# Optimization experiments

Measured on AMD Instinct MI355X. Metric: run time of the kernel, lower is better.

## Reference

```python
import jax, jax.numpy as jnp
import numpy as np

DIM = 2048
N_HEADS = 32
N_KV_HEADS = 8
HEAD_DIM = 64
N_REP = N_HEADS // N_KV_HEADS
SEQ = 2048
BATCH = 1


def _llama3_scaled_rope(head_dim, end, base=10000.0, scale_factor=8):
    # matches executorch precompute_freqs_cis with use_scaled=True
    freqs = 1.0 / (base ** (np.arange(0, head_dim, 2)[: head_dim // 2] / head_dim))
    low_freq_factor, high_freq_factor, old_ctx = 1.0, 4.0, 8192.0
    low_wl = old_ctx / low_freq_factor
    high_wl = old_ctx / high_freq_factor
    wavelen = 2.0 * np.pi / freqs
    smooth = (old_ctx / wavelen - low_freq_factor) / (high_freq_factor - low_freq_factor)
    scaled = np.where(
        wavelen < high_wl,
        freqs,
        np.where(wavelen > low_wl, freqs / scale_factor,
                 (1.0 - smooth) * freqs / scale_factor + smooth * freqs),
    )
    t = np.arange(end, dtype=np.float64)
    ang = np.outer(t, scaled)
    return np.cos(ang).astype(np.float32), np.sin(ang).astype(np.float32)


def setup_inputs() -> dict:
    key = jax.random.key(0)
    kx, kq, kk, kv, ko = jax.random.split(key, 5)
    x = jax.random.normal(kx, (BATCH, SEQ, DIM), dtype=jnp.float32)
    sc = 0.02
    wq = jax.random.normal(kq, (N_HEADS * HEAD_DIM, DIM), dtype=jnp.float32) * sc
    wk = jax.random.normal(kk, (N_KV_HEADS * HEAD_DIM, DIM), dtype=jnp.float32) * sc
    wv = jax.random.normal(kv, (N_KV_HEADS * HEAD_DIM, DIM), dtype=jnp.float32) * sc
    wo = jax.random.normal(ko, (N_HEADS * HEAD_DIM, DIM), dtype=jnp.float32).T * sc
    cos, sin = _llama3_scaled_rope(HEAD_DIM, SEQ)
    return {"x": x, "freqs_cos": jnp.asarray(cos), "freqs_sin": jnp.asarray(sin),
            "wq": wq, "wk": wk, "wv": wv, "wo": wo}


def _apply_rotary(x, cos, sin):
    # x: [b, s, h, hd]; cos/sin: [s, hd//2]; interleaved-pair RoPE
    xr = x[..., 0::2]
    xi = x[..., 1::2]
    c = cos[None, :, None, :]
    s = sin[None, :, None, :]
    out_r = xr * c - xi * s
    out_i = xr * s + xi * c
    return jnp.stack([out_r, out_i], axis=-1).reshape(x.shape)


def reference(x, freqs_cos, freqs_sin, wq, wk, wv, wo):
    b, s, _ = x.shape
    q = (x @ wq.T).reshape(b, s, N_HEADS, HEAD_DIM)
    k = (x @ wk.T).reshape(b, s, N_KV_HEADS, HEAD_DIM)
    v = (x @ wv.T).reshape(b, s, N_KV_HEADS, HEAD_DIM)
    q = _apply_rotary(q, freqs_cos, freqs_sin)
    k = _apply_rotary(k, freqs_cos, freqs_sin)
    # [b, h, s, hd]
    q = q.transpose(0, 2, 1, 3)
    k = k.transpose(0, 2, 1, 3)
    v = v.transpose(0, 2, 1, 3)
    # GQA: repeat_interleave over head dim
    k = jnp.repeat(k, N_REP, axis=1)
    v = jnp.repeat(v, N_REP, axis=1)
    scale = 1.0 / jnp.sqrt(jnp.asarray(HEAD_DIM, dtype=x.dtype))
    scores = jnp.einsum("bhqd,bhkd->bhqk", q, k) * scale
    causal = jnp.tril(jnp.ones((s, s), dtype=bool))
    scores = jnp.where(causal[None, None], scores, jnp.finfo(scores.dtype).min)
    attn = jax.nn.softmax(scores, axis=-1)
    y = jnp.einsum("bhqk,bhkd->bhqd", attn, v)
    y = y.transpose(0, 2, 1, 3).reshape(b, s, N_HEADS * HEAD_DIM)
    return y @ wo.T
```

## Files before the change

kernel.cpp:

```cpp
#include <hip/hip_runtime.h>
#include <hip/hip_bf16.h>

typedef __attribute__((ext_vector_type(8))) __bf16 bf16x8;
typedef __attribute__((ext_vector_type(4))) __bf16 bf16x4;
typedef __attribute__((ext_vector_type(4))) float f32x4;

#define DIM 2048
#define SEQ 2048
#define NH 32
#define NKV 8
#define HD 64
#define QKVD 3072
#define KOFF 2048
#define VOFF 2560
#define KVDIM 512

__device__ __forceinline__ void gld16(const __bf16* g, __bf16* l) {
    __builtin_amdgcn_global_load_lds(
        (const __attribute__((address_space(1))) void*)g,
        (__attribute__((address_space(3))) void*)l, 16, 0, 0);
}

__global__ void cvt_f32_bf16(const float* __restrict__ in, __bf16* __restrict__ out, int n4) {
    int i = blockIdx.x * blockDim.x + threadIdx.x;
    if (i < n4) {
        float4 v = reinterpret_cast<const float4*>(in)[i];
        bf16x4 o;
        o[0] = (__bf16)v.x; o[1] = (__bf16)v.y; o[2] = (__bf16)v.z; o[3] = (__bf16)v.w;
        reinterpret_cast<bf16x4*>(out)[i] = o;
    }
}

__global__ __launch_bounds__(256) void transpose_v(const __bf16* __restrict__ V,
                                                   __bf16* __restrict__ VT) {
    __shared__ __bf16 t[64][72];
    const int tid = threadIdx.x;
    const int r = tid >> 2, c0 = (tid & 3) * 16;
    const int sb = blockIdx.x * 64;
    const int db = blockIdx.y * 64;
    bf16x8 a0 = *reinterpret_cast<const bf16x8*>(V + (size_t)(sb + r) * QKVD + db + c0);
    bf16x8 a1 = *reinterpret_cast<const bf16x8*>(V + (size_t)(sb + r) * QKVD + db + c0 + 8);
#pragma unroll
    for (int e = 0; e < 8; ++e) { t[c0 + e][r] = a0[e]; t[c0 + 8 + e][r] = a1[e]; }
    __syncthreads();
    bf16x8 o0 = *reinterpret_cast<const bf16x8*>(&t[r][c0]);
    bf16x8 o1 = *reinterpret_cast<const bf16x8*>(&t[r][c0 + 8]);
    *reinterpret_cast<bf16x8*>(VT + (size_t)(db + r) * SEQ + sb + c0) = o0;
    *reinterpret_cast<bf16x8*>(VT + (size_t)(db + r) * SEQ + sb + c0 + 8) = o1;
}

template <typename OutT, bool ROPE>
__global__ __launch_bounds__(256) void gemm_tn(const __bf16* __restrict__ A,
                                               const __bf16* __restrict__ B,
                                               OutT* __restrict__ C,
                                               int M, int N, int K,
                                               float scale, int scaleNlim,
                                               const float* __restrict__ fc,
                                               const float* __restrict__ fs) {
    __shared__ __align__(16) __bf16 As[2][2][128 * 32];
    __shared__ __align__(16) __bf16 Bs[2][2][64 * 32];
    const int tid = threadIdx.x;
    const int lane = tid & 63;
    const int w = tid >> 6;
    const int l15 = lane & 15, lhi = lane >> 4;
    const int mb = blockIdx.y * 128;
    const int nb = blockIdx.x * 64;
    const int wm = (w >> 1) * 64, wn = (w & 1) * 32;

    const int srow = lane >> 2, scol = (lane & 3) * 8;
    const __bf16* gA0 = A + (size_t)(mb + w * 16 + srow) * K + scol;
    const __bf16* gA1 = A + (size_t)(mb + (w + 4) * 16 + srow) * K + scol;
    const __bf16* gB0 = B + (size_t)(nb + w * 16 + srow) * K + scol;

    auto stage = [&](int kk, int buf) {
#pragma unroll
        for (int s = 0; s < 2; ++s) {
            gld16(gA0 + kk + s * 32, As[buf][s] + w * 512);
            gld16(gA1 + kk + s * 32, As[buf][s] + (w + 4) * 512);
            gld16(gB0 + kk + s * 32, Bs[buf][s] + w * 512);
        }
    };

    stage(0, 0);
    __syncthreads();

    f32x4 acc[4][2] = {};
    int cur = 0;
    for (int kk = 0; kk < K; kk += 64, cur ^= 1) {
        if (kk + 64 < K) stage(kk + 64, cur ^ 1);
#pragma unroll
        for (int s = 0; s < 2; ++s) {
            bf16x8 a[4], b[2];
#pragma unroll
            for (int i = 0; i < 4; ++i)
                a[i] = *reinterpret_cast<const bf16x8*>(&As[cur][s][(wm + i * 16 + l15) * 32 + lhi * 8]);
#pragma unroll
            for (int j = 0; j < 2; ++j)
                b[j] = *reinterpret_cast<const bf16x8*>(&Bs[cur][s][(wn + j * 16 + l15) * 32 + lhi * 8]);
#pragma unroll
            for (int i = 0; i < 4; ++i)
#pragma unroll
                for (int j = 0; j < 2; ++j)
                    acc[i][j] = __builtin_amdgcn_mfma_f32_16x16x32_bf16(a[i], b[j], acc[i][j], 0, 0, 0);
        }
        __syncthreads();
    }

    const float sc = (nb < scaleNlim) ? scale : 1.0f;
    const bool doRope = ROPE && (nb < VOFF);
#pragma unroll
    for (int i = 0; i < 4; ++i)
#pragma unroll
        for (int j = 0; j < 2; ++j)
#pragma unroll
            for (int r = 0; r < 4; ++r) {
                float v = acc[i][j][r] * sc;
                if (doRope) {
                    const int col = nb + wn + j * 16 + l15;
                    const int row = mb + wm + i * 16 + lhi * 4 + r;
                    const float vp = __shfl_xor(v, 1);
                    const int fi = (col & 63) >> 1;
                    const float cc = fc[row * 32 + fi];
                    const float ss = fs[row * 32 + fi];
                    v = (col & 1) ? (vp * ss + v * cc) : (v * cc - vp * ss);
                }
                C[(size_t)(mb + wm + i * 16 + lhi * 4 + r) * N + nb + wn + j * 16 + l15] = (OutT)v;
            }
}

__global__ __launch_bounds__(256) void attn_kernel(const __bf16* __restrict__ QKV,
                                                   const __bf16* __restrict__ VT,
                                                   __bf16* __restrict__ Y) {
    const int bx = blockIdx.x;
    const int p = bx >> 5;
    const int h = bx & 31;
    const int kvh = h >> 2;
    const int tid = threadIdx.x;
    const int lane = tid & 63;
    const int w = tid >> 6;
    const int l15 = lane & 15, lhi = lane >> 4;

    __shared__ __align__(16) __bf16 Kl[2][128 * 64];
    __shared__ __align__(16) __bf16 Vl[2][64 * 128];
    __shared__ __align__(16) __bf16 Pl[4][16 * 128];

    const __bf16* Qp = QKV + h * HD;
    const __bf16* Kp = QKV + KOFF + kvh * HD;
    const __bf16* Vth = VT + (size_t)(kvh * HD) * SEQ;

    const int ksr = lane >> 3;
    const int ksc = ((lane & 7) ^ ksr) * 8;
    const int vsr = lane >> 4;

    auto stage = [&](int jt, int buf) {
        const int kvb = jt * 128;
#pragma unroll
        for (int c = 0; c < 4; ++c) {
            const int rb = w * 32 + c * 8;
            gld16(Kp + (size_t)(kvb + rb + ksr) * QKVD + ksc, &Kl[buf][rb * 64]);
        }
#pragma unroll
        for (int c = 0; c < 4; ++c) {
            const int db = w * 16 + c * 4;
            const int row = db + vsr;
            const int col = ((lane & 15) ^ (row & 7)) * 8;
            gld16(Vth + (size_t)row * SEQ + kvb + col, &Vl[buf][db * 128]);
        }
    };

    const int pkey = (l15 & 7) << 2;

    for (int seg = 0; seg < 2; ++seg) {
        const int qt = seg ? (31 - p) : p;
        const int qb = qt * 64;
        const int nkt = (qt + 2) >> 1;
        const int qrow = qb + w * 16 + l15;

        const __bf16* qptr = Qp + (size_t)qrow * QKVD;
        bf16x8 qf0 = *reinterpret_cast<const bf16x8*>(qptr + lhi * 8);
        bf16x8 qf1 = *reinterpret_cast<const bf16x8*>(qptr + 32 + lhi * 8);

        f32x4 o[4] = {};
        float mrun = -1e30f;
        float lpart = 0.f;

        stage(0, 0);
        __syncthreads();

        int cur = 0;
        for (int j = 0; j < nkt; ++j, cur ^= 1) {
            const bool pre = (j + 1 < nkt);
            if (pre) stage(j + 1, cur ^ 1);

            f32x4 sacc[8];
            __builtin_amdgcn_s_setprio(1);
#pragma unroll
            for (int t = 0; t < 8; ++t) {
                const int row = t * 16 + l15;
                const int key = row & 7;
                bf16x8 kf0 = *reinterpret_cast<const bf16x8*>(
                    &Kl[cur][row * 64 + ((lhi ^ key) * 8)]);
                bf16x8 kf1 = *reinterpret_cast<const bf16x8*>(
                    &Kl[cur][row * 64 + (((4 + lhi) ^ key) * 8)]);
                f32x4 z = {0.f, 0.f, 0.f, 0.f};
                z = __builtin_amdgcn_mfma_f32_16x16x32_bf16(kf0, qf0, z, 0, 0, 0);
                z = __builtin_amdgcn_mfma_f32_16x16x32_bf16(kf1, qf1, z, 0, 0, 0);
                sacc[t] = z;
            }
            __builtin_amdgcn_s_setprio(0);

            if (j == nkt - 1) {
#pragma unroll
                for (int t = 0; t < 8; ++t)
#pragma unroll
                    for (int r = 0; r < 4; ++r) {
                        const int kv = j * 128 + t * 16 + lhi * 4 + r;
                        if (kv > qrow) sacc[t][r] = -1e30f;
                    }
            }

            float mt[8];
#pragma unroll
            for (int t = 0; t < 8; ++t)
                mt[t] = fmaxf(fmaxf(sacc[t][0], sacc[t][1]),
                              fmaxf(sacc[t][2], sacc[t][3]));
            float pm = fmaxf(fmaxf(fmaxf(mt[0], mt[1]), fmaxf(mt[2], mt[3])),
                             fmaxf(fmaxf(mt[4], mt[5]), fmaxf(mt[6], mt[7])));

            if (!__all(pm - mrun <= 8.0f)) {
                float full = pm;
                full = fmaxf(full, __shfl_xor(full, 16));
                full = fmaxf(full, __shfl_xor(full, 32));
                const float mn = fmaxf(mrun, full);
                const float a = exp2f(mrun - mn);
                mrun = mn;
                lpart *= a;
                float ar[4];
#pragma unroll
                for (int r = 0; r < 4; ++r) ar[r] = __shfl(a, lhi * 4 + r);
#pragma unroll
                for (int t = 0; t < 4; ++t)
#pragma unroll
                    for (int r = 0; r < 4; ++r) o[t][r] *= ar[r];
            }

#pragma unroll
            for (int t = 0; t < 8; ++t) {
                bf16x4 pk;
#pragma unroll
                for (int r = 0; r < 4; ++r) {
                    const float pv = exp2f(sacc[t][r] - mrun);
                    lpart += pv;
                    pk[r] = (__bf16)pv;
                }
                const int sw = (t * 4 + lhi) ^ pkey;
                *reinterpret_cast<bf16x4*>(&Pl[w][l15 * 128 + sw * 4]) = pk;
            }

            bf16x8 pf[4];
#pragma unroll
            for (int c = 0; c < 4; ++c) {
                const int s0 = (c * 8 + lhi * 2) ^ pkey;
                pf[c] = *reinterpret_cast<const bf16x8*>(&Pl[w][l15 * 128 + s0 * 4]);
            }
            __builtin_amdgcn_s_setprio(1);
#pragma unroll
            for (int t = 0; t < 4; ++t) {
                const int row = t * 16 + l15;
                const int key = row & 7;
#pragma unroll
                for (int c = 0; c < 4; ++c) {
                    bf16x8 vf = *reinterpret_cast<const bf16x8*>(
                        &Vl[cur][row * 128 + (((c * 4 + lhi) ^ key) * 8)]);
                    o[t] = __builtin_amdgcn_mfma_f32_16x16x32_bf16(pf[c], vf, o[t], 0, 0, 0);
                }
            }
            __builtin_amdgcn_s_setprio(0);

            __syncthreads();
        }

        float ls = lpart;
        ls += __shfl_xor(ls, 16);
        ls += __shfl_xor(ls, 32);
        float lr[4];
#pragma unroll
        for (int r = 0; r < 4; ++r) lr[r] = __shfl(ls, lhi * 4 + r);
#pragma unroll
        for (int t = 0; t < 4; ++t)
#pragma unroll
            for (int r = 0; r < 4; ++r) {
                const float val = o[t][r] / lr[r];
                Y[(size_t)(qb + w * 16 + lhi * 4 + r) * DIM + h * HD + t * 16 + l15] =
                    (__bf16)val;
            }
    }
}

extern "C" void kernel_launch(void* const* d_in, const int* in_sizes, int n_in,
                              void* d_out, int out_size, void* d_ws, size_t ws_size,
                              hipStream_t stream) {
    const float* x    = (const float*)d_in[0];
    const float* fcos = (const float*)d_in[1];
    const float* fsin = (const float*)d_in[2];
    const float* wq   = (const float*)d_in[3];
    const float* wk   = (const float*)d_in[4];
    const float* wv   = (const float*)d_in[5];
    const float* wo   = (const float*)d_in[6];
    float* out = (float*)d_out;

    __bf16* xb    = (__bf16*)d_ws;
    __bf16* wqkvb = xb + (size_t)SEQ * DIM;
    __bf16* wob   = wqkvb + (size_t)QKVD * DIM;
    __bf16* QKVb  = wob + (size_t)DIM * DIM;
    __bf16* Yb    = QKVb + (size_t)SEQ * QKVD;
    __bf16* VTb   = Yb + (size_t)SEQ * DIM;

    const int nx  = SEQ * DIM / 4;
    const int nw  = DIM * DIM / 4;
    const int nkv = KVDIM * DIM / 4;
    cvt_f32_bf16<<<(nx + 255) / 256, 256, 0, stream>>>(x, xb, nx);
    cvt_f32_bf16<<<(nw + 255) / 256, 256, 0, stream>>>(wq, wqkvb, nw);
    cvt_f32_bf16<<<(nkv + 255) / 256, 256, 0, stream>>>(wk, wqkvb + (size_t)KOFF * DIM, nkv);
    cvt_f32_bf16<<<(nkv + 255) / 256, 256, 0, stream>>>(wv, wqkvb + (size_t)VOFF * DIM, nkv);
    cvt_f32_bf16<<<(nw + 255) / 256, 256, 0, stream>>>(wo, wob, nw);

    gemm_tn<__bf16, true><<<dim3(QKVD / 64, SEQ / 128), 256, 0, stream>>>(
        xb, wqkvb, QKVb, SEQ, QKVD, DIM, 0.125f * 1.4426950408889634f, KOFF, fcos, fsin);

    transpose_v<<<dim3(SEQ / 64, KVDIM / 64), 256, 0, stream>>>(QKVb + VOFF, VTb);

    attn_kernel<<<dim3(512), 256, 0, stream>>>(QKVb, VTb, Yb);

    gemm_tn<float, false><<<dim3(DIM / 64, SEQ / 128), 256, 0, stream>>>(
        Yb, wob, out, SEQ, DIM, DIM, 1.0f, 0, nullptr, nullptr);
}
```

Measured before the change: 151.0 us.

## Split attention into one q-tile per block with 64-wide KV tiles

Each attention block now handles a single 64-row query tile instead of a paired causal segment. The grid doubles to 1024 blocks, ordered so that heavy tiles are scheduled first. KV tiles shrink from 128 to 64 keys, which halves the LDS footprint, and launch bounds request 4 blocks per CU. This aims to improve occupancy and load balance, and the causal mask now wastes less work on the diagonal tile. In exchange there are more loop iterations, more barriers, and Q is reloaded per block.

```diff
diff --git a/kernel.cpp b/kernel.cpp
--- a/kernel.cpp
+++ b/kernel.cpp
@@ -128,173 +128,160 @@
             }
 }
 
-__global__ __launch_bounds__(256) void attn_kernel(const __bf16* __restrict__ QKV,
-                                                   const __bf16* __restrict__ VT,
-                                                   __bf16* __restrict__ Y) {
+__global__ __launch_bounds__(256, 4) void attn_kernel(const __bf16* __restrict__ QKV,
+                                                      const __bf16* __restrict__ VT,
+                                                      __bf16* __restrict__ Y) {
     const int bx = blockIdx.x;
-    const int p = bx >> 5;
+    const int g = bx >> 8;
+    const int a = (bx >> 5) & 7;
     const int h = bx & 31;
+    const int qt = (g == 0) ? 31 - a : (g == 1) ? a : (g == 2) ? 23 - a : 8 + a;
     const int kvh = h >> 2;
     const int tid = threadIdx.x;
     const int lane = tid & 63;
     const int w = tid >> 6;
     const int l15 = lane & 15, lhi = lane >> 4;
 
-    __shared__ __align__(16) __bf16 Kl[2][128 * 64];
-    __shared__ __align__(16) __bf16 Vl[2][64 * 128];
-    __shared__ __align__(16) __bf16 Pl[4][16 * 128];
+    __shared__ __align__(16) __bf16 Kl[2][64 * 64];
+    __shared__ __align__(16) __bf16 Vl[2][64 * 64];
+    __shared__ __align__(16) __bf16 Pl[4][16 * 64];
 
     const __bf16* Qp = QKV + h * HD;
     const __bf16* Kp = QKV + KOFF + kvh * HD;
     const __bf16* Vth = VT + (size_t)(kvh * HD) * SEQ;
 
-    const int ksr = lane >> 3;
-    const int ksc = ((lane & 7) ^ ksr) * 8;
-    const int vsr = lane >> 4;
+    const int sr = lane >> 3;
+    const int ksc = ((lane & 7) ^ sr) * 8;
+    const int rswz = (l15 & 7);
 
     auto stage = [&](int jt, int buf) {
-        const int kvb = jt * 128;
-#pragma unroll
-        for (int c = 0; c < 4; ++c) {
-            const int rb = w * 32 + c * 8;
-            gld16(Kp + (size_t)(kvb + rb + ksr) * QKVD + ksc, &Kl[buf][rb * 64]);
-        }
-#pragma unroll
-        for (int c = 0; c < 4; ++c) {
-            const int db = w * 16 + c * 4;
-            const int row = db + vsr;
-            const int col = ((lane & 15) ^ (row & 7)) * 8;
-            gld16(Vth + (size_t)row * SEQ + kvb + col, &Vl[buf][db * 128]);
+        const int kvb = jt * 64;
+#pragma unroll
+        for (int c = 0; c < 2; ++c) {
+            const int row = w * 16 + c * 8;
+            gld16(Kp + (size_t)(kvb + row + sr) * QKVD + ksc, &Kl[buf][row * 64]);
+            gld16(Vth + (size_t)(row + sr) * SEQ + kvb + ksc, &Vl[buf][row * 64]);
         }
     };
 
-    const int pkey = (l15 & 7) << 2;
-
-    for (int seg = 0; seg < 2; ++seg) {
-        const int qt = seg ? (31 - p) : p;
-        const int qb = qt * 64;
-        const int nkt = (qt + 2) >> 1;
-        const int qrow = qb + w * 16 + l15;
-
-        const __bf16* qptr = Qp + (size_t)qrow * QKVD;
-        bf16x8 qf0 = *reinterpret_cast<const bf16x8*>(qptr + lhi * 8);
-        bf16x8 qf1 = *reinterpret_cast<const bf16x8*>(qptr + 32 + lhi * 8);
-
-        f32x4 o[4] = {};
-        float mrun = -1e30f;
-        float lpart = 0.f;
-
-        stage(0, 0);
+    const int qb = qt * 64;
+    const int qrow = qb + w * 16 + l15;
+
+    const __bf16* qptr = Qp + (size_t)qrow * QKVD;
+    bf16x8 qf0 = *reinterpret_cast<const bf16x8*>(qptr + lhi * 8);
+    bf16x8 qf1 = *reinterpret_cast<const bf16x8*>(qptr + 32 + lhi * 8);
+
+    f32x4 o[4] = {};
+    float mrun = -1e30f;
+    float lpart = 0.f;
+
+    const int pkey = (l15 & 7) << 1;
+
+    stage(0, 0);
+    __syncthreads();
+
+    int cur = 0;
+    for (int j = 0; j <= qt; ++j, cur ^= 1) {
+        const bool pre = (j < qt);
+        if (pre) stage(j + 1, cur ^ 1);
+
+        f32x4 sacc[4];
+        __builtin_amdgcn_s_setprio(1);
+#pragma unroll
+        for (int t = 0; t < 4; ++t) {
+            const int rb = (t * 16 + l15) * 64;
+            bf16x8 kf0 = *reinterpret_cast<const bf16x8*>(
+                &Kl[cur][rb + ((lhi ^ rswz) * 8)]);
+            bf16x8 kf1 = *reinterpret_cast<const bf16x8*>(
+                &Kl[cur][rb + (((4 + lhi) ^ rswz) * 8)]);
+            f32x4 z = {0.f, 0.f, 0.f, 0.f};
+            z = __builtin_amdgcn_mfma_f32_16x16x32_bf16(kf0, qf0, z, 0, 0, 0);
+            z = __builtin_amdgcn_mfma_f32_16x16x32_bf16(kf1, qf1, z, 0, 0, 0);
+            sacc[t] = z;
+        }
+        __builtin_amdgcn_s_setprio(0);
+
+        if (j == qt) {
+#pragma unroll
+            for (int t = 0; t < 4; ++t)
+#pragma unroll
+                for (int r = 0; r < 4; ++r) {
+                    const int kv = j * 64 + t * 16 + lhi * 4 + r;
+                    if (kv > qrow) sacc[t][r] = -1e30f;
+                }
+        }
+
+        float mt[4];
+#pragma unroll
+        for (int t = 0; t < 4; ++t)
+            mt[t] = fmaxf(fmaxf(sacc[t][0], sacc[t][1]),
+                          fmaxf(sacc[t][2], sacc[t][3]));
+        const float pm = fmaxf(fmaxf(mt[0], mt[1]), fmaxf(mt[2], mt[3]));
+
+        if (!__all(pm - mrun <= 8.0f)) {
+            float full = pm;
+            full = fmaxf(full, __shfl_xor(full, 16));
+            full = fmaxf(full, __shfl_xor(full, 32));
+            const float mn = fmaxf(mrun, full);
+            const float aa = exp2f(mrun - mn);
+            mrun = mn;
+            lpart *= aa;
+            float ar[4];
+#pragma unroll
+            for (int r = 0; r < 4; ++r) ar[r] = __shfl(aa, lhi * 4 + r);
+#pragma unroll
+            for (int t = 0; t < 4; ++t)
+#pragma unroll
+                for (int r = 0; r < 4; ++r) o[t][r] *= ar[r];
+        }
+
+#pragma unroll
+        for (int t = 0; t < 4; ++t) {
+            bf16x4 pk;
+#pragma unroll
+            for (int r = 0; r < 4; ++r) {
+                const float pv = exp2f(sacc[t][r] - mrun);
+                lpart += pv;
+                pk[r] = (__bf16)pv;
+            }
+            const int sw = (t * 4 + lhi) ^ pkey;
+            *reinterpret_cast<bf16x4*>(&Pl[w][l15 * 64 + sw * 4]) = pk;
+        }
+
+        bf16x8 pf0 = *reinterpret_cast<const bf16x8*>(
+            &Pl[w][l15 * 64 + (((lhi * 2) ^ pkey) * 4)]);
+        bf16x8 pf1 = *reinterpret_cast<const bf16x8*>(
+            &Pl[w][l15 * 64 + (((8 + lhi * 2) ^ pkey) * 4)]);
+        __builtin_amdgcn_s_setprio(1);
+#pragma unroll
+        for (int t = 0; t < 4; ++t) {
+            const int rb = (t * 16 + l15) * 64;
+            bf16x8 vf0 = *reinterpret_cast<const bf16x8*>(
+                &Vl[cur][rb + ((lhi ^ rswz) * 8)]);
+            bf16x8 vf1 = *reinterpret_cast<const bf16x8*>(
+                &Vl[cur][rb + (((4 + lhi) ^ rswz) * 8)]);
+            o[t] = __builtin_amdgcn_mfma_f32_16x16x32_bf16(pf0, vf0, o[t], 0, 0, 0);
+            o[t] = __builtin_amdgcn_mfma_f32_16x16x32_bf16(pf1, vf1, o[t], 0, 0, 0);
+        }
+        __builtin_amdgcn_s_setprio(0);
+
         __syncthreads();
-
-        int cur = 0;
-        for (int j = 0; j < nkt; ++j, cur ^= 1) {
-            const bool pre = (j + 1 < nkt);
-            if (pre) stage(j + 1, cur ^ 1);
-
-            f32x4 sacc[8];
-            __builtin_amdgcn_s_setprio(1);
-#pragma unroll
-            for (int t = 0; t < 8; ++t) {
-                const int row = t * 16 + l15;
-                const int key = row & 7;
-                bf16x8 kf0 = *reinterpret_cast<const bf16x8*>(
-                    &Kl[cur][row * 64 + ((lhi ^ key) * 8)]);
-                bf16x8 kf1 = *reinterpret_cast<const bf16x8*>(
-                    &Kl[cur][row * 64 + (((4 + lhi) ^ key) * 8)]);
-                f32x4 z = {0.f, 0.f, 0.f, 0.f};
-                z = __builtin_amdgcn_mfma_f32_16x16x32_bf16(kf0, qf0, z, 0, 0, 0);
-                z = __builtin_amdgcn_mfma_f32_16x16x32_bf16(kf1, qf1, z, 0, 0, 0);
-                sacc[t] = z;
-            }
-            __builtin_amdgcn_s_setprio(0);
-
-            if (j == nkt - 1) {
-#pragma unroll
-                for (int t = 0; t < 8; ++t)
-#pragma unroll
-                    for (int r = 0; r < 4; ++r) {
-                        const int kv = j * 128 + t * 16 + lhi * 4 + r;
-                        if (kv > qrow) sacc[t][r] = -1e30f;
-                    }
-            }
-
-            float mt[8];
-#pragma unroll
-            for (int t = 0; t < 8; ++t)
-                mt[t] = fmaxf(fmaxf(sacc[t][0], sacc[t][1]),
-                              fmaxf(sacc[t][2], sacc[t][3]));
-            float pm = fmaxf(fmaxf(fmaxf(mt[0], mt[1]), fmaxf(mt[2], mt[3])),
-                             fmaxf(fmaxf(mt[4], mt[5]), fmaxf(mt[6], mt[7])));
-
-            if (!__all(pm - mrun <= 8.0f)) {
-                float full = pm;
-                full = fmaxf(full, __shfl_xor(full, 16));
-                full = fmaxf(full, __shfl_xor(full, 32));
-                const float mn = fmaxf(mrun, full);
-                const float a = exp2f(mrun - mn);
-                mrun = mn;
-                lpart *= a;
-                float ar[4];
-#pragma unroll
-                for (int r = 0; r < 4; ++r) ar[r] = __shfl(a, lhi * 4 + r);
-#pragma unroll
-                for (int t = 0; t < 4; ++t)
-#pragma unroll
-                    for (int r = 0; r < 4; ++r) o[t][r] *= ar[r];
-            }
-
-#pragma unroll
-            for (int t = 0; t < 8; ++t) {
-                bf16x4 pk;
-#pragma unroll
-                for (int r = 0; r < 4; ++r) {
-                    const float pv = exp2f(sacc[t][r] - mrun);
-                    lpart += pv;
-                    pk[r] = (__bf16)pv;
-                }
-                const int sw = (t * 4 + lhi) ^ pkey;
-                *reinterpret_cast<bf16x4*>(&Pl[w][l15 * 128 + sw * 4]) = pk;
-            }
-
-            bf16x8 pf[4];
-#pragma unroll
-            for (int c = 0; c < 4; ++c) {
-                const int s0 = (c * 8 + lhi * 2) ^ pkey;
-                pf[c] = *reinterpret_cast<const bf16x8*>(&Pl[w][l15 * 128 + s0 * 4]);
-            }
-            __builtin_amdgcn_s_setprio(1);
-#pragma unroll
-            for (int t = 0; t < 4; ++t) {
-                const int row = t * 16 + l15;
-                const int key = row & 7;
-#pragma unroll
-                for (int c = 0; c < 4; ++c) {
-                    bf16x8 vf = *reinterpret_cast<const bf16x8*>(
-                        &Vl[cur][row * 128 + (((c * 4 + lhi) ^ key) * 8)]);
-                    o[t] = __builtin_amdgcn_mfma_f32_16x16x32_bf16(pf[c], vf, o[t], 0, 0, 0);
-                }
-            }
-            __builtin_amdgcn_s_setprio(0);
-
-            __syncthreads();
-        }
-
-        float ls = lpart;
-        ls += __shfl_xor(ls, 16);
-        ls += __shfl_xor(ls, 32);
-        float lr[4];
-#pragma unroll
-        for (int r = 0; r < 4; ++r) lr[r] = __shfl(ls, lhi * 4 + r);
-#pragma unroll
-        for (int t = 0; t < 4; ++t)
-#pragma unroll
-            for (int r = 0; r < 4; ++r) {
-                const float val = o[t][r] / lr[r];
-                Y[(size_t)(qb + w * 16 + lhi * 4 + r) * DIM + h * HD + t * 16 + l15] =
-                    (__bf16)val;
-            }
     }
+
+    float ls = lpart;
+    ls += __shfl_xor(ls, 16);
+    ls += __shfl_xor(ls, 32);
+    float lr[4];
+#pragma unroll
+    for (int r = 0; r < 4; ++r) lr[r] = __shfl(ls, lhi * 4 + r);
+#pragma unroll
+    for (int t = 0; t < 4; ++t)
+#pragma unroll
+        for (int r = 0; r < 4; ++r) {
+            const float val = o[t][r] / lr[r];
+            Y[(size_t)(qb + w * 16 + lhi * 4 + r) * DIM + h * HD + t * 16 + l15] =
+                (__bf16)val;
+        }
 }
 
 extern "C" void kernel_launch(void* const* d_in, const int* in_sizes, int n_in,
@@ -330,7 +317,7 @@
 
     transpose_v<<<dim3(SEQ / 64, KVDIM / 64), 256, 0, stream>>>(QKVb + VOFF, VTb);
 
-    attn_kernel<<<dim3(512), 256, 0, stream>>>(QKVb, VTb, Yb);
+    attn_kernel<<<dim3(1024), 256, 0, stream>>>(QKVb, VTb, Yb);
 
     gemm_tn<float, false><<<dim3(DIM / 64, SEQ / 128), 256, 0, stream>>>(
         Yb, wob, out, SEQ, DIM, DIM, 1.0f, 0, nullptr, nullptr);
```

Result: faster. 145.8 us (-3.5%).
